# Kernel optimization log

Measured on AMD Instinct MI355X. Metric: run time of the kernel, lower is better.

## Reference

```python
import jax, jax.numpy as jnp
import numpy as np

SIGMA = 2.0


def _level(h, centers, W, b):
    # h: [n_prev, d], centers: [n_cur, d], W: [d, d] (torch Linear weight), b: [d]
    # squared distances via expansion: ||h||^2 - 2 h.c + ||c||^2  -> [n_prev, n_cur]
    sq = (jnp.sum(h * h, axis=1, keepdims=True)
          - 2.0 * (h @ centers.T)
          + jnp.sum(centers * centers, axis=1)[None, :])
    p = jax.nn.softmax(-sq / (2.0 * SIGMA), axis=1)  # softmax over centers per row
    t = jnp.tanh(h @ W.T + b)                        # [n_prev, d]
    # h_next[i] = sum_j p[j, i] * t[j]
    return p.T @ t                                   # [n_cur, d]


def setup_inputs() -> dict:
    key = jax.random.key(0)
    ks = jax.random.split(key, 11)
    d = 1024
    num_centers = [16384, 2048, 256, 32]
    inp = {"task_embedding": jax.random.normal(ks[0], (num_centers[0], d), dtype=jnp.float32)}
    # cluster centers per level (torch.rand -> uniform [0,1))
    inp["centers1"] = jax.random.uniform(ks[1], (num_centers[1], d), dtype=jnp.float32)
    inp["centers2"] = jax.random.uniform(ks[2], (num_centers[2], d), dtype=jnp.float32)
    inp["centers3"] = jax.random.uniform(ks[3], (num_centers[3], d), dtype=jnp.float32)
    # linear layers (Kaiming-uniform-ish init bound)
    bound = 1.0 / np.sqrt(d)
    for i, kw, kb in [(1, ks[4], ks[5]), (2, ks[6], ks[7]), (3, ks[8], ks[9])]:
        inp[f"W{i}"] = jax.random.uniform(kw, (d, d), minval=-bound, maxval=bound, dtype=jnp.float32)
        inp[f"b{i}"] = jax.random.uniform(kb, (d,), minval=-bound, maxval=bound, dtype=jnp.float32)
    return inp


def reference(task_embedding, centers1, centers2, centers3, W1, b1, W2, b2, W3, b3):
    h = task_embedding
    h = _level(h, centers1, W1, b1)
    h = _level(h, centers2, W2, b2)
    h = _level(h, centers3, W3, b3)
    return h
```

## Files before the change

kernel.cpp:

```cpp
#include <hip/hip_runtime.h>
#include <cmath>

typedef _Float16 half8 __attribute__((ext_vector_type(8)));
typedef _Float16 half4v __attribute__((ext_vector_type(4)));
typedef __attribute__((ext_vector_type(4))) float floatx4;

#define GLOAD_LDS16(gp, lp)                                            \
  __builtin_amdgcn_global_load_lds(                                    \
      (const __attribute__((address_space(1))) void*)(gp),             \
      (__attribute__((address_space(3))) void*)(lp), 16, 0, 0)

static inline int cdiv(int a, int b) { return (a + b - 1) / b; }

__global__ void prep(const float* __restrict__ h0, const float* __restrict__ W1,
                     const float* __restrict__ W2, const float* __restrict__ W3,
                     const float* __restrict__ c1, const float* __restrict__ c2,
                     const float* __restrict__ c3,
                     _Float16* __restrict__ hh, _Float16* __restrict__ Wh1,
                     _Float16* __restrict__ Wh2, _Float16* __restrict__ Wh3,
                     _Float16* __restrict__ cb1, _Float16* __restrict__ cb2,
                     _Float16* __restrict__ cb3,
                     float* __restrict__ cn1, float* __restrict__ cn2,
                     float* __restrict__ cn3,
                     int nh, int nw, int castBlocks, int n1, int n2) {
  int t = threadIdx.x;
  if ((int)blockIdx.x < castBlocks) {
    int gi = (blockIdx.x * 256 + t) * 4;
    const float* src; _Float16* dst; int off;
    if (gi < nh)                { src = h0; dst = hh;  off = gi; }
    else if (gi < nh + nw)      { src = W1; dst = Wh1; off = gi - nh; }
    else if (gi < nh + 2 * nw)  { src = W2; dst = Wh2; off = gi - nh - nw; }
    else if (gi < nh + 3 * nw)  { src = W3; dst = Wh3; off = gi - nh - 2 * nw; }
    else return;
    float4 v = *(const float4*)(src + off);
    half4v o = {(_Float16)v.x, (_Float16)v.y, (_Float16)v.z, (_Float16)v.w};
    *(half4v*)(dst + off) = o;
    return;
  }
  int row = blockIdx.x - castBlocks;
  const float* c; _Float16* cb; float* cn;
  if (row < n1)            { c = c1; cb = cb1; cn = cn1; }
  else if (row < n1 + n2)  { row -= n1; c = c2; cb = cb2; cn = cn2; }
  else                     { row -= n1 + n2; c = c3; cb = cb3; cn = cn3; }
  float4 v = *(const float4*)(c + (size_t)row * 1024 + t * 4);
  half4v o = {(_Float16)v.x, (_Float16)v.y, (_Float16)v.z, (_Float16)v.w};
  *(half4v*)(cb + (size_t)row * 1024 + t * 4) = o;
  float s = v.x * v.x + v.y * v.y + v.z * v.z + v.w * v.w;
  #pragma unroll
  for (int off = 32; off > 0; off >>= 1) s += __shfl_down(s, off, 64);
  __shared__ float ws[4];
  if ((t & 63) == 0) ws[t >> 6] = s;
  __syncthreads();
  if (t == 0) cn[row] = ws[0] + ws[1] + ws[2] + ws[3];
}

#define SM_CHUNK 64
__global__ void colexp_partial(_Float16* __restrict__ ST, const float* __restrict__ pmax,
                               float* __restrict__ psum, int mchunks, int ncur, int nprev) {
  int col = (blockIdx.x * 256 + threadIdx.x) * 4;
  if (col >= nprev) return;
  float m0 = -1e30f, m1 = -1e30f, m2 = -1e30f, m3 = -1e30f;
  for (int k = 0; k < mchunks; ++k) {
    float4 v = *(const float4*)(pmax + (size_t)k * nprev + col);
    m0 = fmaxf(m0, v.x); m1 = fmaxf(m1, v.y); m2 = fmaxf(m2, v.z); m3 = fmaxf(m3, v.w);
  }
  int j0 = blockIdx.y * SM_CHUNK;
  int j1 = min(j0 + SM_CHUNK, ncur);
  float s0 = 0.f, s1 = 0.f, s2 = 0.f, s3 = 0.f;
  for (int j = j0; j < j1; ++j) {
    size_t o = (size_t)j * nprev + col;
    half4v x = *(const half4v*)(ST + o);
    float e0 = __expf((float)x[0] - m0), e1 = __expf((float)x[1] - m1);
    float e2 = __expf((float)x[2] - m2), e3 = __expf((float)x[3] - m3);
    half4v e = {(_Float16)e0, (_Float16)e1, (_Float16)e2, (_Float16)e3};
    *(half4v*)(ST + o) = e;
    s0 += e0; s1 += e1; s2 += e2; s3 += e3;
  }
  float4 sv = {s0, s1, s2, s3};
  *(float4*)(psum + (size_t)blockIdx.y * nprev + col) = sv;
}

__global__ void reduce_parts(const _Float16* __restrict__ part, _Float16* __restrict__ out,
                             int mn, int S) {
  int i = (blockIdx.x * 256 + threadIdx.x) * 4;
  if (i >= mn) return;
  float a0 = 0.f, a1 = 0.f, a2 = 0.f, a3 = 0.f;
  for (int s = 0; s < S; ++s) {
    half4v v = *(const half4v*)(part + (size_t)s * mn + i);
    a0 += (float)v[0]; a1 += (float)v[1]; a2 += (float)v[2]; a3 += (float)v[3];
  }
  half4v o = {(_Float16)a0, (_Float16)a1, (_Float16)a2, (_Float16)a3};
  *(half4v*)(out + i) = o;
}

enum { EP_LOGIT = 0, EP_TANH = 1, EP_TANHP = 2, EP_F16 = 3, EP_F32 = 4, EP_PART = 5 };

template<int BM, int BN, int EPI>
__launch_bounds__(256, 4)
__global__ void gemm_nt(const _Float16* __restrict__ A,
                        const _Float16* __restrict__ B,
                        void* __restrict__ Cout,
                        const float* __restrict__ aux1,
                        const float* __restrict__ aux2,
                        float* __restrict__ pmax,
                        int pnchunks,
                        int M, int N, int K, int kLen) {
  constexpr int BK = 64;
  constexpr int WTM = BM / 2, WTN = BN / 2;
  constexpr int FM = WTM / 16, FN = WTN / 16;
  __shared__ __align__(16) _Float16 As[BM * BK];
  __shared__ __align__(16) _Float16 Bs[BN * BK];
  float* smf = (float*)As;
  const int tid  = threadIdx.x;
  const int lane = tid & 63;
  const int wave = tid >> 6;
  const int wm = wave >> 1, wn = wave & 1;
  const int mBase = blockIdx.x * BM, nBase = blockIdx.y * BN;
  const int kBase = blockIdx.z * kLen;
  const int lr    = lane & 15;
  const int kHalf = (lane >> 4) << 3;

  const int srOff  = lane >> 3;
  const int schunk = (lane & 7) ^ srOff;
  floatx4 acc[FM][FN] = {};
  constexpr int AV = BM * BK / (256 * 8);
  constexpr int BV = BN * BK / (256 * 8);

  for (int k0 = kBase; k0 < kBase + kLen; k0 += BK) {
    #pragma unroll
    for (int v = 0; v < AV; ++v) {
      int rowBase = v * 32 + wave * 8;
      int gm = mBase + rowBase + srOff;
      if (gm >= M) gm = M - 1;
      GLOAD_LDS16(A + (size_t)gm * K + k0 + schunk * 8, &As[rowBase * BK]);
    }
    #pragma unroll
    for (int v = 0; v < BV; ++v) {
      int rowBase = v * 32 + wave * 8;
      int gn = nBase + rowBase + srOff;
      if (gn >= N) gn = N - 1;
      GLOAD_LDS16(B + (size_t)gn * K + k0 + schunk * 8, &Bs[rowBase * BK]);
    }
    __syncthreads();
    #pragma unroll
    for (int kk = 0; kk < BK; kk += 32) {
      const int q = (kk + kHalf) >> 3;
      half8 af[FM], bfv[FN];
      #pragma unroll
      for (int i = 0; i < FM; ++i) {
        int r = wm * WTM + i * 16 + lr;
        af[i] = *(const half8*)(&As[r * BK + ((q ^ (r & 7)) << 3)]);
      }
      #pragma unroll
      for (int j = 0; j < FN; ++j) {
        int r = wn * WTN + j * 16 + lr;
        bfv[j] = *(const half8*)(&Bs[r * BK + ((q ^ (r & 7)) << 3)]);
      }
      #pragma unroll
      for (int i = 0; i < FM; ++i)
        #pragma unroll
        for (int j = 0; j < FN; ++j)
          acc[i][j] = __builtin_amdgcn_mfma_f32_16x16x32_f16(af[i], bfv[j], acc[i][j], 0, 0, 0);
    }
    __syncthreads();
  }

  if (EPI == EP_TANH) {
    if (tid < BN) {
      int col = nBase + tid;
      float ssum = 0.f;
      if (col < N)
        for (int k = 0; k < pnchunks; ++k) ssum += aux2[(size_t)k * N + col];
      smf[tid] = 1.f / ssum;
    }
    __syncthreads();
  }

  const int rBase = (lane >> 4) << 2;
  float lmax[FN];
  #pragma unroll
  for (int j = 0; j < FN; ++j) lmax[j] = -1e30f;
  #pragma unroll
  for (int i = 0; i < FM; ++i) {
    #pragma unroll
    for (int j = 0; j < FN; ++j) {
      #pragma unroll
      for (int r = 0; r < 4; ++r) {
        int row = mBase + wm * WTM + i * 16 + rBase + r;
        int col = nBase + wn * WTN + j * 16 + lr;
        if (row < M && col < N) {
          float v = acc[i][j][r];
          size_t o = (size_t)row * N + col;
          if (EPI == EP_LOGIT) {
            v = 0.5f * v - 0.25f * aux1[row];
            ((_Float16*)Cout)[o] = (_Float16)v;
            lmax[j] = fmaxf(lmax[j], v);
          } else if (EPI == EP_TANH) {
            v = tanhf(v + aux1[row]) * smf[col - nBase];
            ((_Float16*)Cout)[o] = (_Float16)v;
          } else if (EPI == EP_TANHP) {
            v = tanhf(v + aux1[row]);
            ((_Float16*)Cout)[o] = (_Float16)v;
          } else if (EPI == EP_F16) {
            ((_Float16*)Cout)[o] = (_Float16)v;
          } else if (EPI == EP_PART) {
            ((_Float16*)Cout)[(size_t)blockIdx.z * M * N + o] = (_Float16)v;
          } else {
            ((float*)Cout)[o] = v;
          }
        }
      }
    }
  }
  if (EPI == EP_LOGIT) {
    #pragma unroll
    for (int j = 0; j < FN; ++j) {
      float m = lmax[j];
      m = fmaxf(m, __shfl_xor(m, 16, 64));
      m = fmaxf(m, __shfl_xor(m, 32, 64));
      if ((lane >> 4) == 0) smf[wm * BN + wn * WTN + j * 16 + lr] = m;
    }
    __syncthreads();
    if (tid < BN) {
      int col = nBase + tid;
      if (col < N)
        pmax[(size_t)blockIdx.x * N + col] = fmaxf(smf[tid], smf[BN + tid]);
    }
  }
}

template<int BM, int BN>
__launch_bounds__(256, 2)
__global__ void fused_ls(const _Float16* __restrict__ A,
                         const _Float16* __restrict__ B,
                         _Float16* __restrict__ Eout,
                         const float* __restrict__ cn,
                         int M, int N, int K) {
  constexpr int BK = 64;
  constexpr int WTM = BM / 2, WTN = BN / 2;
  constexpr int FM = WTM / 16, FN = WTN / 16;
  constexpr int TLD = BN + 4;
  constexpr int STAGE_B = (BM + BN) * BK * 2;
  constexpr int TILE_B  = BM * TLD * 4;
  constexpr int SM_B = STAGE_B > TILE_B ? STAGE_B : TILE_B;
  __shared__ __align__(16) char smem[SM_B];
  _Float16* As = (_Float16*)smem;
  _Float16* Bs = As + BM * BK;
  float* tile = (float*)smem;
  __shared__ float redm[256], reds[256];
  const int tid  = threadIdx.x;
  const int lane = tid & 63;
  const int wave = tid >> 6;
  const int wm = wave >> 1, wn = wave & 1;
  const int nBase = blockIdx.x * BN;
  const int lr    = lane & 15;
  const int kHalf = (lane >> 4) << 3;
  const int srOff  = lane >> 3;
  const int schunk = (lane & 7) ^ srOff;
  floatx4 acc[FM][FN] = {};
  constexpr int AV = BM * BK / (256 * 8);
  constexpr int BV = BN * BK / (256 * 8);

  for (int k0 = 0; k0 < K; k0 += BK) {
    #pragma unroll
    for (int v = 0; v < AV; ++v) {
      int rowBase = v * 32 + wave * 8;
      GLOAD_LDS16(A + (size_t)(rowBase + srOff) * K + k0 + schunk * 8, &As[rowBase * BK]);
    }
    #pragma unroll
    for (int v = 0; v < BV; ++v) {
      int rowBase = v * 32 + wave * 8;
      GLOAD_LDS16(B + (size_t)(nBase + rowBase + srOff) * K + k0 + schunk * 8, &Bs[rowBase * BK]);
    }
    __syncthreads();
    #pragma unroll
    for (int kk = 0; kk < BK; kk += 32) {
      const int q = (kk + kHalf) >> 3;
      half8 af[FM], bfv[FN];
      #pragma unroll
      for (int i = 0; i < FM; ++i) {
        int r = wm * WTM + i * 16 + lr;
        af[i] = *(const half8*)(&As[r * BK + ((q ^ (r & 7)) << 3)]);
      }
      #pragma unroll
      for (int j = 0; j < FN; ++j) {
        int r = wn * WTN + j * 16 + lr;
        bfv[j] = *(const half8*)(&Bs[r * BK + ((q ^ (r & 7)) << 3)]);
      }
      #pragma unroll
      for (int i = 0; i < FM; ++i)
        #pragma unroll
        for (int j = 0; j < FN; ++j)
          acc[i][j] = __builtin_amdgcn_mfma_f32_16x16x32_f16(af[i], bfv[j], acc[i][j], 0, 0, 0);
    }
    __syncthreads();
  }

  const int rBase = (lane >> 4) << 2;
  #pragma unroll
  for (int i = 0; i < FM; ++i)
    #pragma unroll
    for (int j = 0; j < FN; ++j)
      #pragma unroll
      for (int r = 0; r < 4; ++r) {
        int row = wm * WTM + i * 16 + rBase + r;
        int col = wn * WTN + j * 16 + lr;
        tile[row * TLD + col] = 0.5f * acc[i][j][r] - 0.25f * cn[row];
      }
  __syncthreads();

  constexpr int P = 256 / BN;
  const int c = tid & (BN - 1);
  const int p = tid / BN;
  float m = -1e30f;
  for (int j = p; j < M; j += P) m = fmaxf(m, tile[j * TLD + c]);
  redm[p * BN + c] = m;
  __syncthreads();
  float mf = redm[c];
  #pragma unroll
  for (int q = 1; q < P; ++q) mf = fmaxf(mf, redm[q * BN + c]);
  float s = 0.f;
  for (int j = p; j < M; j += P) {
    float e = __expf(tile[j * TLD + c] - mf);
    tile[j * TLD + c] = e;
    s += e;
  }
  reds[p * BN + c] = s;
  __syncthreads();
  float l = 0.f;
  #pragma unroll
  for (int q = 0; q < P; ++q) l += reds[q * BN + c];
  const float li = 1.f / l;
  for (int j = p; j < M; j += P)
    Eout[(size_t)j * N + nBase + c] = (_Float16)(tile[j * TLD + c] * li);
}

template<int EPI>
static int launch_gemm(int M, int N, int K, const _Float16* A, const _Float16* B,
                       void* C, const float* a1, const float* a2, float* pmax,
                       int pnchunks, hipStream_t s) {
  long b128   = (long)cdiv(M, 128) * cdiv(N, 128);
  long b12864 = (long)cdiv(M, 128) * cdiv(N, 64);
  if (b128 >= 192) {
    gemm_nt<128, 128, EPI><<<dim3(cdiv(M, 128), cdiv(N, 128)), 256, 0, s>>>(
        A, B, C, a1, a2, pmax, pnchunks, M, N, K, K);
    return 128;
  } else if (M >= 128 && b12864 >= 192) {
    gemm_nt<128, 64, EPI><<<dim3(cdiv(M, 128), cdiv(N, 64)), 256, 0, s>>>(
        A, B, C, a1, a2, pmax, pnchunks, M, N, K, K);
    return 128;
  } else {
    gemm_nt<64, 64, EPI><<<dim3(cdiv(M, 64), cdiv(N, 64)), 256, 0, s>>>(
        A, B, C, a1, a2, pmax, pnchunks, M, N, K, K);
    return 64;
  }
}

static void launch_gemm_splitk(int M, int N, int K, int S,
                               const _Float16* A, const _Float16* B,
                               _Float16* Cpart, _Float16* Cout, hipStream_t s) {
  int kLen = K / S;
  long b128 = (long)cdiv(M, 128) * cdiv(N, 128) * S;
  if (M >= 128 && N >= 128 && b128 >= 256) {
    gemm_nt<128, 128, EP_PART><<<dim3(cdiv(M, 128), cdiv(N, 128), S), 256, 0, s>>>(
        A, B, Cpart, nullptr, nullptr, nullptr, 0, M, N, K, kLen);
  } else {
    gemm_nt<64, 64, EP_PART><<<dim3(cdiv(M, 64), cdiv(N, 64), S), 256, 0, s>>>(
        A, B, Cpart, nullptr, nullptr, nullptr, 0, M, N, K, kLen);
  }
  int mn = M * N;
  reduce_parts<<<cdiv(mn, 1024), 256, 0, s>>>(Cpart, Cout, mn, S);
}

extern "C" void kernel_launch(void* const* d_in, const int* in_sizes, int n_in,
                              void* d_out, int out_size, void* d_ws, size_t ws_size,
                              hipStream_t stream) {
  const float* h0 = (const float*)d_in[0];
  const float* c1 = (const float*)d_in[1];
  const float* c2 = (const float*)d_in[2];
  const float* c3 = (const float*)d_in[3];
  const float* W1 = (const float*)d_in[4];
  const float* b1 = (const float*)d_in[5];
  const float* W2 = (const float*)d_in[6];
  const float* b2 = (const float*)d_in[7];
  const float* W3 = (const float*)d_in[8];
  const float* b3 = (const float*)d_in[9];

  const int d = 1024;
  const int N0 = 16384, N1 = 2048, N2 = 256, N3 = 32;

  char* w = (char*)d_ws;
  size_t off = 0;
  auto alloc = [&](size_t bytes) {
    void* p = w + off;
    off += (bytes + 255) & ~(size_t)255;
    return p;
  };
  _Float16* hb  = (_Float16*)alloc((size_t)N0 * d * 2);
  _Float16* cb1 = (_Float16*)alloc((size_t)N1 * d * 2);
  _Float16* cb2 = (_Float16*)alloc((size_t)N2 * d * 2);
  _Float16* cb3 = (_Float16*)alloc((size_t)N3 * d * 2);
  float* cn1 = (float*)alloc((size_t)N1 * 4);
  float* cn2 = (float*)alloc((size_t)N2 * 4);
  float* cn3 = (float*)alloc((size_t)N3 * 4);
  _Float16* Wb1 = (_Float16*)alloc((size_t)d * d * 2);
  _Float16* Wb2 = (_Float16*)alloc((size_t)d * d * 2);
  _Float16* Wb3 = (_Float16*)alloc((size_t)d * d * 2);
  _Float16* ST = (_Float16*)alloc((size_t)N1 * N0 * 2);
  _Float16* tT = (_Float16*)alloc((size_t)d * N0 * 2);
  float* pmax = (float*)alloc((size_t)32 * N0 * 4);
  float* psum = (float*)alloc((size_t)32 * N0 * 4);
  _Float16* h1b = (_Float16*)alloc((size_t)N1 * d * 2);
  _Float16* h2b = (_Float16*)alloc((size_t)N2 * d * 2);
  _Float16* Cpart = (_Float16*)alloc((size_t)8 * N1 * d * 2);
  _Float16* E = ST;
  (void)ws_size; (void)in_sizes; (void)n_in; (void)out_size;

  int nh = N0 * d, nw = d * d;
  int castBlocks = cdiv(nh + 3 * nw, 1024);
  prep<<<castBlocks + N1 + N2 + N3, 256, 0, stream>>>(
      h0, W1, W2, W3, c1, c2, c3, hb, Wb1, Wb2, Wb3, cb1, cb2, cb3,
      cn1, cn2, cn3, nh, nw, castBlocks, N1, N2);

  int bm = launch_gemm<EP_LOGIT>(N1, N0, d, cb1, hb, ST, cn1, nullptr, pmax, 0, stream);
  colexp_partial<<<dim3(N0 / 1024, cdiv(N1, SM_CHUNK)), 256, 0, stream>>>(
      ST, pmax, psum, cdiv(N1, bm), N1, N0);
  launch_gemm<EP_TANH>(d, N0, d, Wb1, hb, tT, b1, psum, nullptr, cdiv(N1, SM_CHUNK), stream);
  launch_gemm_splitk(N1, d, N0, 8, E, tT, Cpart, h1b, stream);

  fused_ls<256, 64><<<N1 / 64, 256, 0, stream>>>(cb2, h1b, E, cn2, N2, N1, d);
  launch_gemm<EP_TANHP>(d, N1, d, Wb2, h1b, tT, b2, nullptr, nullptr, 0, stream);
  launch_gemm_splitk(N2, d, N1, 8, E, tT, Cpart, h2b, stream);

  fused_ls<32, 64><<<N2 / 64, 256, 0, stream>>>(cb3, h2b, E, cn3, N3, N2, d);
  launch_gemm<EP_TANHP>(d, N2, d, Wb3, h2b, tT, b3, nullptr, nullptr, 0, stream);
  launch_gemm<EP_F32>(N3, d, N2, E, tT, d_out, nullptr, nullptr, nullptr, 0, stream);
}
```

Measured before the change: 492.5 us.

## Fuse level-3 tanh GEMM and output GEMM into one kernel; retile level-2 softmax

Adds a level3_out kernel in which each of 16 blocks computes a 64-column slice of tanh(W3·h2ᵀ+b3) in LDS, then immediately multiplies it by the level-3 softmax weights to write the final fp32 output. This replaces two separate GEMM launches and the global round trip of the intermediate tanh matrix. The level-2 fused_ls launch also moves from 64 to 32 columns per block, doubling the block count. The fused kernel uses only 16 workgroups, so it leaves most of the GPU idle; the intent is to trade that for less launch overhead and less memory traffic on a tiny tail stage.

```diff
diff --git a/kernel.cpp b/kernel.cpp
--- a/kernel.cpp
+++ b/kernel.cpp
@@ -335,6 +335,97 @@
     Eout[(size_t)j * N + nBase + c] = (_Float16)(tile[j * TLD + c] * li);
 }
 
+__launch_bounds__(256)
+__global__ void level3_out(const _Float16* __restrict__ W3h,
+                           const _Float16* __restrict__ h2,
+                           const _Float16* __restrict__ E3,
+                           const float* __restrict__ b3,
+                           float* __restrict__ out) {
+  constexpr int BK = 64, K = 1024, NI = 256, MO = 32, NS = 64;
+  constexpr int T3LD = NI + 8;
+  __shared__ __align__(16) _Float16 smem[(NS + NI) * BK];
+  _Float16* As = smem;
+  _Float16* Bs = smem + NS * BK;
+  _Float16* t3 = smem;
+  const int tid  = threadIdx.x;
+  const int lane = tid & 63;
+  const int wave = tid >> 6;
+  const int wm = wave >> 1, wn = wave & 1;
+  const int n0 = blockIdx.x * NS;
+  const int lr    = lane & 15;
+  const int kHalf = (lane >> 4) << 3;
+  const int srOff  = lane >> 3;
+  const int schunk = (lane & 7) ^ srOff;
+  const int rBase = (lane >> 4) << 2;
+
+  floatx4 acc[2][8] = {};
+  for (int k0 = 0; k0 < K; k0 += BK) {
+    #pragma unroll
+    for (int v = 0; v < 2; ++v) {
+      int rowBase = v * 32 + wave * 8;
+      GLOAD_LDS16(W3h + (size_t)(n0 + rowBase + srOff) * K + k0 + schunk * 8, &As[rowBase * BK]);
+    }
+    #pragma unroll
+    for (int v = 0; v < 8; ++v) {
+      int rowBase = v * 32 + wave * 8;
+      GLOAD_LDS16(h2 + (size_t)(rowBase + srOff) * K + k0 + schunk * 8, &Bs[rowBase * BK]);
+    }
+    __syncthreads();
+    #pragma unroll
+    for (int kk = 0; kk < BK; kk += 32) {
+      const int q = (kk + kHalf) >> 3;
+      half8 af[2], bfv[8];
+      #pragma unroll
+      for (int i = 0; i < 2; ++i) {
+        int r = wm * 32 + i * 16 + lr;
+        af[i] = *(const half8*)(&As[r * BK + ((q ^ (r & 7)) << 3)]);
+      }
+      #pragma unroll
+      for (int j = 0; j < 8; ++j) {
+        int r = wn * 128 + j * 16 + lr;
+        bfv[j] = *(const half8*)(&Bs[r * BK + ((q ^ (r & 7)) << 3)]);
+      }
+      #pragma unroll
+      for (int i = 0; i < 2; ++i)
+        #pragma unroll
+        for (int j = 0; j < 8; ++j)
+          acc[i][j] = __builtin_amdgcn_mfma_f32_16x16x32_f16(af[i], bfv[j], acc[i][j], 0, 0, 0);
+    }
+    __syncthreads();
+  }
+  #pragma unroll
+  for (int i = 0; i < 2; ++i)
+    #pragma unroll
+    for (int j = 0; j < 8; ++j)
+      #pragma unroll
+      for (int r = 0; r < 4; ++r) {
+        int n = wm * 32 + i * 16 + rBase + r;
+        int ii = wn * 128 + j * 16 + lr;
+        t3[n * T3LD + ii] = (_Float16)tanhf(acc[i][j][r] + b3[n0 + n]);
+      }
+  __syncthreads();
+
+  floatx4 acc2[2] = {};
+  for (int k0 = 0; k0 < NI; k0 += 32) {
+    half8 af[2];
+    #pragma unroll
+    for (int i = 0; i < 2; ++i)
+      af[i] = *(const half8*)(E3 + (size_t)(i * 16 + lr) * NI + k0 + kHalf);
+    half8 bf = *(const half8*)(&t3[(wave * 16 + lr) * T3LD + k0 + kHalf]);
+    #pragma unroll
+    for (int i = 0; i < 2; ++i)
+      acc2[i] = __builtin_amdgcn_mfma_f32_16x16x32_f16(af[i], bf, acc2[i], 0, 0, 0);
+  }
+  #pragma unroll
+  for (int i = 0; i < 2; ++i)
+    #pragma unroll
+    for (int r = 0; r < 4; ++r) {
+      int j = i * 16 + rBase + r;
+      int n = n0 + wave * 16 + lr;
+      out[(size_t)j * 1024 + n] = acc2[i][r];
+    }
+}
+
 template<int EPI>
 static int launch_gemm(int M, int N, int K, const _Float16* A, const _Float16* B,
                        void* C, const float* a1, const float* a2, float* pmax,
@@ -428,11 +519,10 @@
   launch_gemm<EP_TANH>(d, N0, d, Wb1, hb, tT, b1, psum, nullptr, cdiv(N1, SM_CHUNK), stream);
   launch_gemm_splitk(N1, d, N0, 8, E, tT, Cpart, h1b, stream);
 
-  fused_ls<256, 64><<<N1 / 64, 256, 0, stream>>>(cb2, h1b, E, cn2, N2, N1, d);
+  fused_ls<256, 32><<<N1 / 32, 256, 0, stream>>>(cb2, h1b, E, cn2, N2, N1, d);
   launch_gemm<EP_TANHP>(d, N1, d, Wb2, h1b, tT, b2, nullptr, nullptr, 0, stream);
   launch_gemm_splitk(N2, d, N1, 8, E, tT, Cpart, h2b, stream);
 
   fused_ls<32, 64><<<N2 / 64, 256, 0, stream>>>(cb3, h2b, E, cn3, N3, N2, d);
-  launch_gemm<EP_TANHP>(d, N2, d, Wb3, h2b, tT, b3, nullptr, nullptr, 0, stream);
-  launch_gemm<EP_F32>(N3, d, N2, E, tT, d_out, nullptr, nullptr, nullptr, 0, stream);
-}
+  level3_out<<<16, 256, 0, stream>>>(Wb3, h2b, E, b3, (float*)d_out);
+}
```

Result: no change. 501.9 us (+1.9%).
